# Kernel optimization log

Measured on AMD Instinct MI355X. Metric: run time of the kernel, lower is better.

## Reference

```python
import jax, jax.numpy as jnp
import numpy as np

N_HEADS = 16
DIM = 1024
HW = 32
B = 8


def _conv3x3(x, W, b):
    # x: [B, C, H, W], W: [O, I, 3, 3] (OIHW), padding 1 == SAME for stride 1
    y = jax.lax.conv_general_dilated(
        x, W, window_strides=(1, 1), padding='SAME',
        dimension_numbers=('NCHW', 'OIHW', 'NCHW'))
    return y + b[None, :, None, None]


def setup_inputs() -> dict:
    key = jax.random.key(0)
    ks = jax.random.split(key, 8)
    f32 = jnp.float32
    q = jax.random.normal(ks[0], (B, DIM, HW, HW), f32)
    k = jax.random.normal(ks[1], (B, DIM, HW, HW), f32)
    v = jax.random.normal(ks[2], (B, DIM, HW, HW), f32)
    Wq = jax.random.normal(ks[3], (DIM, DIM, 3, 3), f32) * 0.02
    Wk = jax.random.normal(ks[4], (DIM, DIM, 3, 3), f32) * 0.02
    Wv = jax.random.normal(ks[5], (DIM, DIM, 3, 3), f32) * 0.02
    Wo = jax.random.normal(ks[6], (DIM, DIM), f32) * 0.02
    bq = jnp.zeros((DIM,), f32); bk = jnp.zeros((DIM,), f32)
    bv = jnp.zeros((DIM,), f32); bo = jnp.zeros((DIM,), f32)
    mask = jax.random.randint(ks[7], (B, DIM, DIM), 0, 2, jnp.int32)
    return {'q': q, 'k': k, 'v': v, 'Wq': Wq, 'bq': bq, 'Wk': Wk, 'bk': bk,
            'Wv': Wv, 'bv': bv, 'Wo': Wo, 'bo': bo, 'mask': mask}


def reference(q, k, v, Wq, bq, Wk, bk, Wv, bv, Wo, bo, mask):
    Bq, C, H, W = q.shape  # C == dim, tokens = channels
    h = N_HEADS
    d = (H * W) // h  # head dim

    def split_heads(x):
        # [B, C, H, W] -> [B, h, C, d]
        return x.reshape(Bq, C, h, d).transpose(0, 2, 1, 3)

    qh = split_heads(_conv3x3(q, Wq, bq))
    kh = split_heads(_conv3x3(k, Wk, bk))
    vh = split_heads(_conv3x3(v, Wv, bv))

    scale = 1.0 / np.sqrt(d).astype(np.float32)
    attn = jnp.einsum('bhtd,bhsd->bhts', qh, kh) * scale  # [B, h, C, C]
    attn = jnp.where(mask[:, None, :, :] == 0, jnp.float32(-1e9), attn)
    w = jax.nn.softmax(attn, axis=-1)  # attn_dropout rate = 0 -> identity
    out = jnp.einsum('bhts,bhsd->bhtd', w, vh)  # [B, h, C, d]
    out = out.transpose(0, 2, 1, 3).reshape(Bq, C, h * d)  # [B, C, H*W]
    out = out @ Wo.T + bo  # Linear(dim, dim); H*W == dim
    return out
```

## Files before the change

kernel.cpp:

```cpp
#include <hip/hip_runtime.h>

typedef __attribute__((ext_vector_type(8))) short bh8;
typedef __attribute__((ext_vector_type(4))) short bh4;
typedef __attribute__((ext_vector_type(4))) float f32x4;

__device__ __forceinline__ short f2bf(float f) {
  union { float f; unsigned u; } a; a.f = f;
  unsigned r = a.u + 0x7FFFu + ((a.u >> 16) & 1u);
  return (short)(r >> 16);
}

__device__ __forceinline__ void g2l16(const short* g, short* l) {
  __builtin_amdgcn_global_load_lds(
      (const __attribute__((address_space(1))) void*)g,
      (__attribute__((address_space(3))) void*)l, 16, 0, 0);
}

__global__ __launch_bounds__(256) void zero_halo(short* __restrict__ xP) {
  int z = blockIdx.y;
  short* base = xP + (size_t)z * 1183744;
  int ri = blockIdx.x * 2 + (threadIdx.x >> 7);
  int row;
  if (ri < 34) row = ri;
  else if (ri < 68) row = 1122 + (ri - 34);
  else { int j = ri - 68; int y = (j >> 1) + 1; int x = (j & 1) ? 33 : 0; row = y * 34 + x; }
  int col = (threadIdx.x & 127) * 8;
  bh8 zv = {0, 0, 0, 0, 0, 0, 0, 0};
  *(bh8*)(base + (size_t)row * 1024 + col) = zv;
}

__global__ __launch_bounds__(256) void transpose3(
    const float* __restrict__ q, const float* __restrict__ k, const float* __restrict__ v,
    short* __restrict__ qP, short* __restrict__ kP, short* __restrict__ vP) {
  int z = blockIdx.z; int tensor = z >> 3, b = z & 7;
  const float* src = tensor == 0 ? q : (tensor == 1 ? k : v);
  short* dst = tensor == 0 ? qP : (tensor == 1 ? kP : vP);
  src += (size_t)b * 1048576; dst += (size_t)b * 1183744;
  int row0 = blockIdx.y * 64;
  int col0 = blockIdx.x * 64;
  __shared__ short t[64][72];
  int tid = threadIdx.x;
#pragma unroll
  for (int i = 0; i < 2; ++i) {
    int cid = tid + i * 256;
    int r = cid >> 3, co = (cid & 7) * 8;
    const float* p = src + (size_t)(row0 + r) * 1024 + col0 + co;
    float4 f0 = *(const float4*)(p);
    float4 f1 = *(const float4*)(p + 4);
    t[co + 0][r] = f2bf(f0.x); t[co + 1][r] = f2bf(f0.y);
    t[co + 2][r] = f2bf(f0.z); t[co + 3][r] = f2bf(f0.w);
    t[co + 4][r] = f2bf(f1.x); t[co + 5][r] = f2bf(f1.y);
    t[co + 6][r] = f2bf(f1.z); t[co + 7][r] = f2bf(f1.w);
  }
  __syncthreads();
#pragma unroll
  for (int i = 0; i < 2; ++i) {
    int cid = tid + i * 256;
    int sr = cid >> 3, cc = (cid & 7) * 8;
    bh8 val = *(const bh8*)&t[sr][cc];
    int tok = col0 + sr;
    int pr = ((tok >> 5) + 1) * 34 + (tok & 31) + 1;
    *(bh8*)(dst + (size_t)pr * 1024 + row0 + cc) = val;
  }
}

__global__ __launch_bounds__(256) void wperm3(
    const float* __restrict__ Wq, const float* __restrict__ Wk, const float* __restrict__ Wv,
    short* __restrict__ WpQ, short* __restrict__ WpK, short* __restrict__ WpV) {
  int z = blockIdx.y;
  const float* W = z == 0 ? Wq : (z == 1 ? Wk : Wv);
  short* Wp = z == 0 ? WpQ : (z == 1 ? WpK : WpV);
  int idx = blockIdx.x * 256 + threadIdx.x;
  const float* wsrc = W + (size_t)idx * 9;
#pragma unroll
  for (int t = 0; t < 9; ++t) Wp[(size_t)t * 1048576 + idx] = f2bf(wsrc[t]);
}

__global__ __launch_bounds__(256) void cvt_bf(const float* __restrict__ src,
                                              short* __restrict__ dst) {
  int idx = (blockIdx.x * 256 + threadIdx.x) * 4;
  float4 f = *(const float4*)(src + idx);
  bh4 o; o[0] = f2bf(f.x); o[1] = f2bf(f.y); o[2] = f2bf(f.z); o[3] = f2bf(f.w);
  *(bh4*)(dst + idx) = o;
}

__global__ __launch_bounds__(256) void mask_pack(const int* __restrict__ m,
                                                 unsigned* __restrict__ mp) {
  int idx = blockIdx.x * 256 + threadIdx.x;
  const int* src = m + (size_t)idx * 32;
  unsigned wv = 0;
#pragma unroll
  for (int j = 0; j < 32; j += 4) {
    int4 a = *(const int4*)(src + j);
    wv |= ((unsigned)(a.x & 1) << j) | ((unsigned)(a.y & 1) << (j + 1)) |
          ((unsigned)(a.z & 1) << (j + 2)) | ((unsigned)(a.w & 1) << (j + 3));
  }
  mp[idx] = wv;
}

__global__ __launch_bounds__(256) void conv_gemm_all(
    const short* __restrict__ WpQ, const short* __restrict__ WpK, const short* __restrict__ WpV,
    const short* __restrict__ xPq, const short* __restrict__ xPk, const short* __restrict__ xPv,
    short* __restrict__ cQ, short* __restrict__ cK, short* __restrict__ cVT,
    const float* __restrict__ bq, const float* __restrict__ bk, const float* __restrict__ bv,
    int convSel) {
  __shared__ short sA[4096];
  __shared__ short sB[4096];
  int tid = threadIdx.x, lane = tid & 63, w = tid >> 6;
  int z = blockIdx.z;
  int conv = convSel >= 0 ? convSel : (z >> 3);
  int b = convSel >= 0 ? z : (z & 7);
  const short* Wp = conv == 0 ? WpQ : (conv == 1 ? WpK : WpV);
  const short* xP = conv == 0 ? xPq : (conv == 1 ? xPk : xPv);
  short* out = conv == 0 ? cQ : (conv == 1 ? cK : cVT);
  const float* bias = conv == 0 ? bq : (conv == 1 ? bk : bv);
  int XisA = (conv == 2);
  int mbase = blockIdx.x * 128, nbase = blockIdx.y * 128;
  const short* xb = xP + (size_t)b * 1183744;
  int wbase = XisA ? nbase : mbase;
  int sbase = XisA ? mbase : nbase;
  short* sW = XisA ? sB : sA;
  short* sX = XisA ? sA : sB;

  int colsh = (lane & 3) * 8;
  int ldsoff[2]; const short* wp0[2]; const short* xp0[2];
#pragma unroll
  for (int i = 0; i < 2; ++i) {
    int row = 32 * w + 16 * i + (lane >> 2);
    ldsoff[i] = (2 * w + i) * 512 + lane * 8;
    wp0[i] = Wp + (size_t)(wbase + row) * 1024 + colsh;
    int tok = sbase + row;
    int pr0 = ((tok >> 5) + 1) * 34 + (tok & 31) + 1;
    xp0[i] = xb + (size_t)pr0 * 1024 + colsh;
  }
  f32x4 acc[4][4] = {};
  int wm = (w >> 1) * 64, wn = (w & 1) * 64;
  for (int tap = 0; tap < 9; ++tap) {
    int dOff = (tap / 3 - 1) * 34 + (tap % 3 - 1);
    size_t wtap = (size_t)tap * 1048576;
    for (int kt = 0; kt < 1024; kt += 32) {
#pragma unroll
      for (int i = 0; i < 2; ++i) {
        g2l16(wp0[i] + wtap + kt, sW + ldsoff[i]);
        g2l16(xp0[i] + (ptrdiff_t)dOff * 1024 + kt, sX + ldsoff[i]);
      }
      __syncthreads();
      bh8 af[4], bfr[4];
#pragma unroll
      for (int mt = 0; mt < 4; ++mt)
        af[mt] = *(const bh8*)&sA[(wm + mt * 16 + (lane & 15)) * 32 + (lane >> 4) * 8];
#pragma unroll
      for (int nt = 0; nt < 4; ++nt)
        bfr[nt] = *(const bh8*)&sB[(wn + nt * 16 + (lane & 15)) * 32 + (lane >> 4) * 8];
#pragma unroll
      for (int mt = 0; mt < 4; ++mt)
#pragma unroll
        for (int nt = 0; nt < 4; ++nt)
          acc[mt][nt] = __builtin_amdgcn_mfma_f32_16x16x32_bf16(af[mt], bfr[nt], acc[mt][nt], 0, 0, 0);
      __syncthreads();
    }
  }
  size_t ob = (size_t)b * 1048576;
#pragma unroll
  for (int mt = 0; mt < 4; ++mt) {
#pragma unroll
    for (int nt = 0; nt < 4; ++nt) {
      int m0 = mbase + wm + mt * 16 + ((lane >> 4) << 2);
      int n = nbase + wn + nt * 16 + (lane & 15);
#pragma unroll
      for (int r = 0; r < 4; ++r) {
        float bv = bias[XisA ? n : (m0 + r)];
        out[ob + (size_t)(m0 + r) * 1024 + n] = f2bf(acc[mt][nt][r] + bv);
      }
    }
  }
}

__global__ __launch_bounds__(256) void attn(
    const short* __restrict__ Qc, const short* __restrict__ Kc,
    const short* __restrict__ VT, const unsigned* __restrict__ Mp,
    short* __restrict__ AO) {
  __shared__ short sQ[64][72];
  __shared__ short sK[128][72];
  __shared__ short sV[64][136];
  __shared__ short sP[64][136];
  int tid = threadIdx.x, lane = tid & 63, w = tid >> 6;
  int qbase = blockIdx.x * 64, h = blockIdx.y, b = blockIdx.z;
  int j0 = h * 64;
  const short* Qb = Qc + (size_t)b * 1048576;
  const short* Kb = Kc + (size_t)b * 1048576;
  const short* Vb = VT + (size_t)b * 1048576;
  const unsigned* Mpb = Mp + (size_t)b * 32768;
  const float scale = 0.125f;

#pragma unroll
  for (int i = 0; i < 2; ++i) {
    int cid = tid + i * 256;
    int row = cid >> 3, co = (cid & 7) * 8;
    *(bh8*)&sQ[row][co] = *(const bh8*)(Qb + (size_t)(qbase + row) * 1024 + j0 + co);
  }
  __syncthreads();

  int tg = qbase + w * 16 + (lane & 15);
  int rsel = ((lane >> 4) << 2);
  float mrow = -3.0e38f, lrow = 0.0f;
  f32x4 oacc[4] = {};

  for (int st = 0; st < 8; ++st) {
#pragma unroll
    for (int i = 0; i < 4; ++i) {
      int cid = tid + i * 256;
      int row = cid >> 3, co = (cid & 7) * 8;
      *(bh8*)&sK[row][co] = *(const bh8*)(Kb + (size_t)(st * 128 + row) * 1024 + j0 + co);
      int vrow = cid >> 4, vco = (cid & 15) * 8;
      *(bh8*)&sV[vrow][vco] = *(const bh8*)(Vb + (size_t)(j0 + vrow) * 1024 + st * 128 + vco);
    }
    __syncthreads();

    f32x4 sacc[8];
#pragma unroll
    for (int mt = 0; mt < 8; ++mt) {
      f32x4 a = {0.f, 0.f, 0.f, 0.f};
      bh8 kf = *(const bh8*)&sK[mt * 16 + (lane & 15)][(lane >> 4) * 8];
      bh8 qf = *(const bh8*)&sQ[w * 16 + (lane & 15)][(lane >> 4) * 8];
      a = __builtin_amdgcn_mfma_f32_16x16x32_bf16(kf, qf, a, 0, 0, 0);
      kf = *(const bh8*)&sK[mt * 16 + (lane & 15)][32 + (lane >> 4) * 8];
      qf = *(const bh8*)&sQ[w * 16 + (lane & 15)][32 + (lane >> 4) * 8];
      a = __builtin_amdgcn_mfma_f32_16x16x32_bf16(kf, qf, a, 0, 0, 0);
      sacc[mt] = a;
    }

    uint4 Mw = *(const uint4*)(Mpb + (size_t)tg * 32 + st * 4);
    float tmax = -3.0e38f;
#pragma unroll
    for (int mt = 0; mt < 8; ++mt) {
      unsigned mwv = ((const unsigned*)&Mw)[mt >> 1] >> ((mt & 1) * 16 + rsel);
      f32x4 vv;
      vv[0] = (mwv & 1u) ? sacc[mt][0] * scale : -1e9f;
      vv[1] = (mwv & 2u) ? sacc[mt][1] * scale : -1e9f;
      vv[2] = (mwv & 4u) ? sacc[mt][2] * scale : -1e9f;
      vv[3] = (mwv & 8u) ? sacc[mt][3] * scale : -1e9f;
      sacc[mt] = vv;
      tmax = fmaxf(tmax, fmaxf(fmaxf(vv[0], vv[1]), fmaxf(vv[2], vv[3])));
    }
    tmax = fmaxf(tmax, __shfl_xor(tmax, 16, 64));
    tmax = fmaxf(tmax, __shfl_xor(tmax, 32, 64));
    float mnew = fmaxf(mrow, tmax);
    float alpha = __expf(fminf(mrow - mnew, 0.f));

    float sum = 0.f;
    uint4 Mw2 = Mw;
#pragma unroll
    for (int mt = 0; mt < 8; ++mt) {
      unsigned mwv = ((const unsigned*)&Mw2)[mt >> 1] >> ((mt & 1) * 16 + rsel);
      float p0 = (mwv & 1u) ? __expf(fminf(sacc[mt][0] - mnew, 0.f)) : 0.f;
      float p1 = (mwv & 2u) ? __expf(fminf(sacc[mt][1] - mnew, 0.f)) : 0.f;
      float p2 = (mwv & 4u) ? __expf(fminf(sacc[mt][2] - mnew, 0.f)) : 0.f;
      float p3 = (mwv & 8u) ? __expf(fminf(sacc[mt][3] - mnew, 0.f)) : 0.f;
      sum += (p0 + p1) + (p2 + p3);
      bh4 p; p[0] = f2bf(p0); p[1] = f2bf(p1); p[2] = f2bf(p2); p[3] = f2bf(p3);
      *(bh4*)&sP[w * 16 + (lane & 15)][mt * 16 + rsel] = p;
    }
    sum += __shfl_xor(sum, 16, 64);
    sum += __shfl_xor(sum, 32, 64);
    lrow = lrow * alpha + sum;
    mrow = mnew;

    float al[4];
#pragma unroll
    for (int r = 0; r < 4; ++r) al[r] = __shfl(alpha, rsel + r, 64);
#pragma unroll
    for (int nt = 0; nt < 4; ++nt)
#pragma unroll
      for (int r = 0; r < 4; ++r) oacc[nt][r] *= al[r];
    __syncthreads();

#pragma unroll
    for (int k0 = 0; k0 < 4; ++k0) {
      bh8 pf = *(const bh8*)&sP[w * 16 + (lane & 15)][k0 * 32 + (lane >> 4) * 8];
#pragma unroll
      for (int nt = 0; nt < 4; ++nt) {
        bh8 vf = *(const bh8*)&sV[nt * 16 + (lane & 15)][k0 * 32 + (lane >> 4) * 8];
        oacc[nt] = __builtin_amdgcn_mfma_f32_16x16x32_bf16(pf, vf, oacc[nt], 0, 0, 0);
      }
    }
    __syncthreads();
  }

  float rl[4];
#pragma unroll
  for (int r = 0; r < 4; ++r) rl[r] = 1.0f / __shfl(lrow, rsel + r, 64);
  size_t ob = (size_t)b * 1048576;
#pragma unroll
  for (int nt = 0; nt < 4; ++nt) {
    int j = nt * 16 + (lane & 15);
    int t0 = qbase + w * 16 + rsel;
#pragma unroll
    for (int r = 0; r < 4; ++r)
      AO[ob + (size_t)(t0 + r) * 1024 + j0 + j] = f2bf(oacc[nt][r] * rl[r]);
  }
}

__global__ __launch_bounds__(256) void gemm_bt(
    const short* __restrict__ A, const short* __restrict__ Bm,
    float* __restrict__ out, const float* __restrict__ bias) {
  __shared__ short sA[4096];
  __shared__ short sB[4096];
  int tid = threadIdx.x, lane = tid & 63, w = tid >> 6;
  int mbase = blockIdx.x * 128, nbase = blockIdx.y * 128;
  int colsh = (lane & 3) * 8;
  int ldsoff[2]; const short* ap[2]; const short* bp[2];
#pragma unroll
  for (int i = 0; i < 2; ++i) {
    int row = 32 * w + 16 * i + (lane >> 2);
    ldsoff[i] = (2 * w + i) * 512 + lane * 8;
    ap[i] = A + (size_t)(mbase + row) * 1024 + colsh;
    bp[i] = Bm + (size_t)(nbase + row) * 1024 + colsh;
  }
  f32x4 acc[4][4] = {};
  int wm = (w >> 1) * 64, wn = (w & 1) * 64;
  for (int kt = 0; kt < 1024; kt += 32) {
#pragma unroll
    for (int i = 0; i < 2; ++i) {
      g2l16(ap[i] + kt, sA + ldsoff[i]);
      g2l16(bp[i] + kt, sB + ldsoff[i]);
    }
    __syncthreads();
    bh8 af[4], bfr[4];
#pragma unroll
    for (int mt = 0; mt < 4; ++mt)
      af[mt] = *(const bh8*)&sA[(wm + mt * 16 + (lane & 15)) * 32 + (lane >> 4) * 8];
#pragma unroll
    for (int nt = 0; nt < 4; ++nt)
      bfr[nt] = *(const bh8*)&sB[(wn + nt * 16 + (lane & 15)) * 32 + (lane >> 4) * 8];
#pragma unroll
    for (int mt = 0; mt < 4; ++mt)
#pragma unroll
      for (int nt = 0; nt < 4; ++nt)
        acc[mt][nt] = __builtin_amdgcn_mfma_f32_16x16x32_bf16(af[mt], bfr[nt], acc[mt][nt], 0, 0, 0);
    __syncthreads();
  }
#pragma unroll
  for (int mt = 0; mt < 4; ++mt) {
#pragma unroll
    for (int nt = 0; nt < 4; ++nt) {
      int m0 = mbase + wm + mt * 16 + ((lane >> 4) << 2);
      int n = nbase + wn + nt * 16 + (lane & 15);
      float bv = bias[n];
#pragma unroll
      for (int r = 0; r < 4; ++r)
        out[(size_t)(m0 + r) * 1024 + n] = acc[mt][nt][r] + bv;
    }
  }
}

extern "C" void kernel_launch(void* const* d_in, const int* in_sizes, int n_in,
                              void* d_out, int out_size, void* d_ws, size_t ws_size,
                              hipStream_t stream) {
  (void)in_sizes; (void)n_in; (void)out_size;
  const float* q    = (const float*)d_in[0];
  const float* k    = (const float*)d_in[1];
  const float* v    = (const float*)d_in[2];
  const float* Wq   = (const float*)d_in[3];
  const float* bq   = (const float*)d_in[4];
  const float* Wk   = (const float*)d_in[5];
  const float* bk   = (const float*)d_in[6];
  const float* Wv   = (const float*)d_in[7];
  const float* bv   = (const float*)d_in[8];
  const float* Wo   = (const float*)d_in[9];
  const float* bo   = (const float*)d_in[10];
  const int*   mask = (const int*)d_in[11];
  float* out = (float*)d_out;
  char* ws = (char*)d_ws;

  const size_t XPE = 1156ull * 1024 * 8;
  const size_t XPB = XPE * 2;
  const size_t WPE = 9ull * 1048576;
  short* xPq = (short*)ws;
  short* xPk = xPq + XPE;
  short* xPv = xPk + XPE;
  short* WpQ = (short*)(ws + 3 * XPB);
  short* WpK = WpQ + WPE;
  short* WpV = WpK + WPE;
  char* p2 = ws + 3 * XPB + 3 * WPE * 2;

  bool fused = ws_size >= 167000000ull;
  short *cQ, *cK, *cVT, *WoB, *AO; unsigned* Mpk;
  if (fused) {
    cQ  = (short*)(p2);
    cK  = (short*)(p2 + 16777216);
    cVT = (short*)(p2 + 33554432);
    WoB = (short*)(p2 + 50331648);
    Mpk = (unsigned*)(p2 + 52428800);
    AO  = xPq;
  } else {
    cQ  = (short*)(p2);
    WoB = (short*)(p2 + 16777216);
    Mpk = (unsigned*)(p2 + 18874368);
    cK  = xPq;
    cVT = xPk;
    AO  = xPv;
  }

  zero_halo<<<dim3(66, 24), dim3(256), 0, stream>>>(xPq);
  transpose3<<<dim3(16, 16, 24), dim3(256), 0, stream>>>(q, k, v, xPq, xPk, xPv);
  wperm3<<<dim3(4096, 3), dim3(256), 0, stream>>>(Wq, Wk, Wv, WpQ, WpK, WpV);
  cvt_bf<<<dim3(1024), dim3(256), 0, stream>>>(Wo, WoB);
  mask_pack<<<dim3(1024), dim3(256), 0, stream>>>(mask, Mpk);
  if (fused) {
    conv_gemm_all<<<dim3(8, 8, 24), dim3(256), 0, stream>>>(
        WpQ, WpK, WpV, xPq, xPk, xPv, cQ, cK, cVT, bq, bk, bv, -1);
  } else {
    conv_gemm_all<<<dim3(8, 8, 8), dim3(256), 0, stream>>>(
        WpQ, WpK, WpV, xPq, xPk, xPv, cQ, cK, cVT, bq, bk, bv, 0);
    conv_gemm_all<<<dim3(8, 8, 8), dim3(256), 0, stream>>>(
        WpQ, WpK, WpV, xPq, xPk, xPv, cQ, cK, cVT, bq, bk, bv, 1);
    conv_gemm_all<<<dim3(8, 8, 8), dim3(256), 0, stream>>>(
        WpQ, WpK, WpV, xPq, xPk, xPv, cQ, cK, cVT, bq, bk, bv, 2);
  }
  attn<<<dim3(16, 16, 8), dim3(256), 0, stream>>>(cQ, cK, cVT, Mpk, AO);
  gemm_bt<<<dim3(64, 8), dim3(256), 0, stream>>>(AO, WoB, out, bo);
}
```

Before: 913.8 us.

## Rewrite conv GEMM as 256x256 tile, 4-stage LDS pipeline with swizzle

Replaces the 128x128 single-buffered conv implicit-GEMM with a 512-thread kernel that computes 256x256 tiles. It uses a 4-deep LDS ring of global_load_lds stages with explicit vmcnt waits, raw barriers, and setprio around MFMA bursts. The LDS column layout is XOR-swizzled to avoid bank conflicts, and workgroup IDs are remapped so neighbouring blocks share operands in cache. This aims to hide global load latency and raise arithmetic intensity, which matters because the conv GEMMs dominate runtime. In exchange it uses 128 KB of LDS and many accumulator registers per wave, with a correctness risk from the manual waitcnt accounting.

```diff
diff --git a/kernel.cpp b/kernel.cpp
--- a/kernel.cpp
+++ b/kernel.cpp
@@ -14,6 +14,12 @@
   __builtin_amdgcn_global_load_lds(
       (const __attribute__((address_space(1))) void*)g,
       (__attribute__((address_space(3))) void*)l, 16, 0, 0);
+}
+
+__device__ __forceinline__ void barrier_raw() {
+  asm volatile("" ::: "memory");
+  __builtin_amdgcn_s_barrier();
+  asm volatile("" ::: "memory");
 }
 
 __global__ __launch_bounds__(256) void zero_halo(short* __restrict__ xP) {
@@ -98,16 +104,21 @@
   mp[idx] = wv;
 }
 
-__global__ __launch_bounds__(256) void conv_gemm_all(
+__global__ __launch_bounds__(512, 2) void conv_gemm256(
     const short* __restrict__ WpQ, const short* __restrict__ WpK, const short* __restrict__ WpV,
     const short* __restrict__ xPq, const short* __restrict__ xPk, const short* __restrict__ xPv,
     short* __restrict__ cQ, short* __restrict__ cK, short* __restrict__ cVT,
     const float* __restrict__ bq, const float* __restrict__ bk, const float* __restrict__ bv,
     int convSel) {
-  __shared__ short sA[4096];
-  __shared__ short sB[4096];
-  int tid = threadIdx.x, lane = tid & 63, w = tid >> 6;
-  int z = blockIdx.z;
+  __shared__ short lds[65536];
+  int tid = threadIdx.x, lane = tid & 63, wid = tid >> 6;
+
+  int fid = blockIdx.x + (blockIdx.y << 2) + (blockIdx.z << 4);
+  int nwg = (int)(gridDim.z) << 4;
+  int cpx = nwg >> 3;
+  int swz = (fid & 7) * cpx + (fid >> 3);
+  int mtile = swz & 3, ntile = (swz >> 2) & 3, z = swz >> 4;
+
   int conv = convSel >= 0 ? convSel : (z >> 3);
   int b = convSel >= 0 ? z : (z & 7);
   const short* Wp = conv == 0 ? WpQ : (conv == 1 ? WpK : WpV);
@@ -115,62 +126,119 @@
   short* out = conv == 0 ? cQ : (conv == 1 ? cK : cVT);
   const float* bias = conv == 0 ? bq : (conv == 1 ? bk : bv);
   int XisA = (conv == 2);
-  int mbase = blockIdx.x * 128, nbase = blockIdx.y * 128;
+  int mbase = mtile * 256, nbase = ntile * 256;
   const short* xb = xP + (size_t)b * 1183744;
   int wbase = XisA ? nbase : mbase;
   int sbase = XisA ? mbase : nbase;
-  short* sW = XisA ? sB : sA;
-  short* sX = XisA ? sA : sB;
-
-  int colsh = (lane & 3) * 8;
-  int ldsoff[2]; const short* wp0[2]; const short* xp0[2];
-#pragma unroll
-  for (int i = 0; i < 2; ++i) {
-    int row = 32 * w + 16 * i + (lane >> 2);
-    ldsoff[i] = (2 * w + i) * 512 + lane * 8;
-    wp0[i] = Wp + (size_t)(wbase + row) * 1024 + colsh;
-    int tok = sbase + row;
-    int pr0 = ((tok >> 5) + 1) * 34 + (tok & 31) + 1;
-    xp0[i] = xb + (size_t)pr0 * 1024 + colsh;
-  }
-  f32x4 acc[4][4] = {};
-  int wm = (w >> 1) * 64, wn = (w & 1) * 64;
-  for (int tap = 0; tap < 9; ++tap) {
-    int dOff = (tap / 3 - 1) * 34 + (tap % 3 - 1);
-    size_t wtap = (size_t)tap * 1048576;
-    for (int kt = 0; kt < 1024; kt += 32) {
-#pragma unroll
-      for (int i = 0; i < 2; ++i) {
-        g2l16(wp0[i] + wtap + kt, sW + ldsoff[i]);
-        g2l16(xp0[i] + (ptrdiff_t)dOff * 1024 + kt, sX + ldsoff[i]);
-      }
-      __syncthreads();
-      bh8 af[4], bfr[4];
-#pragma unroll
-      for (int mt = 0; mt < 4; ++mt)
-        af[mt] = *(const bh8*)&sA[(wm + mt * 16 + (lane & 15)) * 32 + (lane >> 4) * 8];
-#pragma unroll
-      for (int nt = 0; nt < 4; ++nt)
-        bfr[nt] = *(const bh8*)&sB[(wn + nt * 16 + (lane & 15)) * 32 + (lane >> 4) * 8];
-#pragma unroll
-      for (int mt = 0; mt < 4; ++mt)
-#pragma unroll
-        for (int nt = 0; nt < 4; ++nt)
-          acc[mt][nt] = __builtin_amdgcn_mfma_f32_16x16x32_bf16(af[mt], bfr[nt], acc[mt][nt], 0, 0, 0);
-      __syncthreads();
-    }
-  }
+
+  int srow = wid * 16 + (lane >> 2);
+  int lsl = (lane & 3) ^ ((lane >> 2) & 3);
+  int gcol = lsl * 8;
+  const short* pW[2]; const short* pX[2];
+#pragma unroll
+  for (int h = 0; h < 2; ++h) {
+    pW[h] = Wp + (size_t)(wbase + h * 128 + srow) * 1024 + gcol;
+    int tok = sbase + h * 128 + srow;
+    int pr = ((tok >> 5) + 1) * 34 + (tok & 31) + 1;
+    pX[h] = xb + (size_t)pr * 1024 + gcol;
+  }
+  const short* pA0 = XisA ? pX[0] : pW[0];
+  const short* pA1 = XisA ? pX[1] : pW[1];
+  const short* pB0 = XisA ? pW[0] : pX[0];
+  const short* pB1 = XisA ? pW[1] : pX[1];
+  int sdst = wid * 512 + lane * 8;
+
+  int pslot = (((lane >> 4) ^ (lane & 3)) << 3);
+  int rdA = ((wid >> 2) * 128 + (lane & 15)) * 32 + pslot;
+  int rdB = 8192 + ((wid & 3) * 64 + (lane & 15)) * 32 + pslot;
+
+  f32x4 acc[8][4] = {};
+  short* stBd = nullptr; const short* stBs0 = nullptr; const short* stBs1 = nullptr;
+
+#pragma unroll
+  for (int u = 0; u < 3; ++u) {
+    ptrdiff_t dW = (ptrdiff_t)(u << 5);
+    ptrdiff_t dX = (ptrdiff_t)(-35) * 1024 + (u << 5);
+    ptrdiff_t dA = XisA ? dX : dW, dB = XisA ? dW : dX;
+    short* du = &lds[u * 16384 + sdst];
+    g2l16(pA0 + dA, du);
+    g2l16(pA1 + dA, du + 4096);
+    g2l16(pB0 + dB, du + 8192);
+    g2l16(pB1 + dB, du + 12288);
+  }
+  asm volatile("s_waitcnt vmcnt(8)" ::: "memory");
+  barrier_raw();
+
+#define CT_MFMA16(ACCROW) \
+    _Pragma("unroll") for (int mm = 0; mm < 4; ++mm) { \
+      _Pragma("unroll") for (int nn = 0; nn < 4; ++nn) \
+        acc[(ACCROW) + mm][nn] = __builtin_amdgcn_mfma_f32_16x16x32_bf16( \
+            afr[mm], bfr[nn], acc[(ACCROW) + mm][nn], 0, 0, 0); \
+    }
+
+#define TILEBODY(REGS, T, DOSTAGE, WSTR) do { \
+    const short* Lp = &lds[(REGS)]; \
+    bh8 afr[4], bfr[4]; \
+    _Pragma("unroll") for (int mm = 0; mm < 4; ++mm) \
+      afr[mm] = *(const bh8*)(Lp + rdA + mm * 512); \
+    _Pragma("unroll") for (int nn = 0; nn < 4; ++nn) \
+      bfr[nn] = *(const bh8*)(Lp + rdB + nn * 512); \
+    if (DOSTAGE) { \
+      int u_ = (T) + 3; \
+      int tap_ = u_ >> 5, kk_ = (u_ & 31) << 5; \
+      int tapr_ = (tap_ * 11) >> 5; \
+      ptrdiff_t dW_ = (ptrdiff_t)tap_ * 1048576 + kk_; \
+      ptrdiff_t dX_ = (ptrdiff_t)(tapr_ * 34 + (tap_ - tapr_ * 3) - 35) * 1024 + kk_; \
+      ptrdiff_t dA_ = XisA ? dX_ : dW_, dB_ = XisA ? dW_ : dX_; \
+      short* du_ = &lds[(u_ & 3) * 16384 + sdst]; \
+      g2l16(pA0 + dA_, du_); \
+      g2l16(pA1 + dA_, du_ + 4096); \
+      stBd = du_ + 8192; stBs0 = pB0 + dB_; stBs1 = pB1 + dB_; \
+    } \
+    barrier_raw(); \
+    __builtin_amdgcn_s_setprio(1); \
+    CT_MFMA16(0) \
+    __builtin_amdgcn_s_setprio(0); \
+    barrier_raw(); \
+    _Pragma("unroll") for (int mm = 0; mm < 4; ++mm) \
+      afr[mm] = *(const bh8*)(Lp + rdA + 2048 + mm * 512); \
+    if (DOSTAGE) { g2l16(stBs0, stBd); g2l16(stBs1, stBd + 4096); } \
+    barrier_raw(); \
+    __builtin_amdgcn_s_setprio(1); \
+    CT_MFMA16(4) \
+    __builtin_amdgcn_s_setprio(0); \
+    asm volatile(WSTR ::: "memory"); \
+    barrier_raw(); \
+  } while (0)
+
+#pragma unroll 1
+  for (int it = 0; it < 71; ++it) {
+    int t0 = it * 4;
+#pragma unroll
+    for (int j = 0; j < 4; ++j) {
+      TILEBODY(j * 16384, t0 + j, true, "s_waitcnt vmcnt(8)");
+    }
+  }
+  TILEBODY(0,     284, true,  "s_waitcnt vmcnt(8)");
+  TILEBODY(16384, 285, false, "s_waitcnt vmcnt(4)");
+  TILEBODY(32768, 286, false, "s_waitcnt vmcnt(0)");
+  TILEBODY(49152, 287, false, "");
+
+#undef TILEBODY
+#undef CT_MFMA16
+
   size_t ob = (size_t)b * 1048576;
-#pragma unroll
-  for (int mt = 0; mt < 4; ++mt) {
-#pragma unroll
-    for (int nt = 0; nt < 4; ++nt) {
-      int m0 = mbase + wm + mt * 16 + ((lane >> 4) << 2);
-      int n = nbase + wn + nt * 16 + (lane & 15);
+  int wr = wid >> 2, wc = wid & 3;
+#pragma unroll
+  for (int m = 0; m < 8; ++m) {
+#pragma unroll
+    for (int n = 0; n < 4; ++n) {
+      int m0 = mbase + wr * 128 + m * 16 + ((lane >> 4) << 2);
+      int nn = nbase + wc * 64 + n * 16 + (lane & 15);
 #pragma unroll
       for (int r = 0; r < 4; ++r) {
-        float bv = bias[XisA ? n : (m0 + r)];
-        out[ob + (size_t)(m0 + r) * 1024 + n] = f2bf(acc[mt][nt][r] + bv);
+        float bvv = bias[XisA ? nn : (m0 + r)];
+        out[ob + (size_t)(m0 + r) * 1024 + nn] = f2bf(acc[m][n][r] + bvv);
       }
     }
   }
@@ -408,14 +476,14 @@
   cvt_bf<<<dim3(1024), dim3(256), 0, stream>>>(Wo, WoB);
   mask_pack<<<dim3(1024), dim3(256), 0, stream>>>(mask, Mpk);
   if (fused) {
-    conv_gemm_all<<<dim3(8, 8, 24), dim3(256), 0, stream>>>(
+    conv_gemm256<<<dim3(4, 4, 24), dim3(512), 0, stream>>>(
         WpQ, WpK, WpV, xPq, xPk, xPv, cQ, cK, cVT, bq, bk, bv, -1);
   } else {
-    conv_gemm_all<<<dim3(8, 8, 8), dim3(256), 0, stream>>>(
+    conv_gemm256<<<dim3(4, 4, 8), dim3(512), 0, stream>>>(
         WpQ, WpK, WpV, xPq, xPk, xPv, cQ, cK, cVT, bq, bk, bv, 0);
-    conv_gemm_all<<<dim3(8, 8, 8), dim3(256), 0, stream>>>(
+    conv_gemm256<<<dim3(4, 4, 8), dim3(512), 0, stream>>>(
         WpQ, WpK, WpV, xPq, xPk, xPv, cQ, cK, cVT, bq, bk, bv, 1);
-    conv_gemm_all<<<dim3(8, 8, 8), dim3(256), 0, stream>>>(
+    conv_gemm256<<<dim3(4, 4, 8), dim3(512), 0, stream>>>(
         WpQ, WpK, WpV, xPq, xPk, xPv, cQ, cK, cVT, bq, bk, bv, 2);
   }
   attn<<<dim3(16, 16, 8), dim3(256), 0, stream>>>(cQ, cK, cVT, Mpk, AO);
```

Result: faster. 891.9 us (-2.4%).

## Rewrite conv GEMM with triple-buffered LDS pipeline, larger tiles and swizzle

Applied to the files above, without the earlier changes.

Replaces the conv implicit-GEMM kernel with a 512-thread, 256x128-tile version. It prefetches two k-steps ahead into three rotating LDS buffers, waits with vmcnt and uses one raw barrier per step. It also XOR-swizzles LDS slots to cut bank conflicts, raises wave priority during MFMAs, and remaps block ids so neighbouring tiles share a chiplet. The aim is to hide global-load latency and cut barrier stalls, at the cost of more LDS per block and lower occupancy.

```diff
diff --git a/kernel.cpp b/kernel.cpp
--- a/kernel.cpp
+++ b/kernel.cpp
@@ -14,6 +14,12 @@
   __builtin_amdgcn_global_load_lds(
       (const __attribute__((address_space(1))) void*)g,
       (__attribute__((address_space(3))) void*)l, 16, 0, 0);
+}
+
+__device__ __forceinline__ void barrier_raw() {
+  asm volatile("" ::: "memory");
+  __builtin_amdgcn_s_barrier();
+  asm volatile("" ::: "memory");
 }
 
 __global__ __launch_bounds__(256) void zero_halo(short* __restrict__ xP) {
@@ -98,16 +104,21 @@
   mp[idx] = wv;
 }
 
-__global__ __launch_bounds__(256) void conv_gemm_all(
+__global__ __launch_bounds__(512, 4) void conv_gemm_td(
     const short* __restrict__ WpQ, const short* __restrict__ WpK, const short* __restrict__ WpV,
     const short* __restrict__ xPq, const short* __restrict__ xPk, const short* __restrict__ xPv,
     short* __restrict__ cQ, short* __restrict__ cK, short* __restrict__ cVT,
     const float* __restrict__ bq, const float* __restrict__ bk, const float* __restrict__ bv,
     int convSel) {
-  __shared__ short sA[4096];
-  __shared__ short sB[4096];
-  int tid = threadIdx.x, lane = tid & 63, w = tid >> 6;
-  int z = blockIdx.z;
+  __shared__ short lds[36864];
+  int tid = threadIdx.x, lane = tid & 63, wid = tid >> 6;
+
+  int fid = blockIdx.x + (blockIdx.y << 2) + ((int)blockIdx.z << 5);
+  int nwg = (int)gridDim.z << 5;
+  int cpx = nwg >> 3;
+  int swz = (fid & 7) * cpx + (fid >> 3);
+  int mtile = swz & 3, ntile = (swz >> 2) & 7, z = swz >> 5;
+
   int conv = convSel >= 0 ? convSel : (z >> 3);
   int b = convSel >= 0 ? z : (z & 7);
   const short* Wp = conv == 0 ? WpQ : (conv == 1 ? WpK : WpV);
@@ -115,62 +126,95 @@
   short* out = conv == 0 ? cQ : (conv == 1 ? cK : cVT);
   const float* bias = conv == 0 ? bq : (conv == 1 ? bk : bv);
   int XisA = (conv == 2);
-  int mbase = blockIdx.x * 128, nbase = blockIdx.y * 128;
+  int mbase = mtile * 256, nbase = ntile * 128;
   const short* xb = xP + (size_t)b * 1183744;
-  int wbase = XisA ? nbase : mbase;
-  int sbase = XisA ? mbase : nbase;
-  short* sW = XisA ? sB : sA;
-  short* sX = XisA ? sA : sB;
-
-  int colsh = (lane & 3) * 8;
-  int ldsoff[2]; const short* wp0[2]; const short* xp0[2];
-#pragma unroll
-  for (int i = 0; i < 2; ++i) {
-    int row = 32 * w + 16 * i + (lane >> 2);
-    ldsoff[i] = (2 * w + i) * 512 + lane * 8;
-    wp0[i] = Wp + (size_t)(wbase + row) * 1024 + colsh;
-    int tok = sbase + row;
-    int pr0 = ((tok >> 5) + 1) * 34 + (tok & 31) + 1;
-    xp0[i] = xb + (size_t)pr0 * 1024 + colsh;
-  }
+
+  int srow = tid >> 2;
+  int lsl = (tid & 3) ^ ((tid >> 3) & 3);
+  int gcol = lsl * 8;
+  const short* pA0; const short* pA1; const short* pB0;
+  if (!XisA) {
+    pA0 = Wp + (size_t)(mbase + srow) * 1024 + gcol;
+    pA1 = Wp + (size_t)(mbase + 128 + srow) * 1024 + gcol;
+    int tok = nbase + srow;
+    pB0 = xb + (size_t)(((tok >> 5) + 1) * 34 + (tok & 31) + 1) * 1024 + gcol;
+  } else {
+    int ta = mbase + srow, tb = mbase + 128 + srow;
+    pA0 = xb + (size_t)(((ta >> 5) + 1) * 34 + (ta & 31) + 1) * 1024 + gcol;
+    pA1 = xb + (size_t)(((tb >> 5) + 1) * 34 + (tb & 31) + 1) * 1024 + gcol;
+    pB0 = Wp + (size_t)(nbase + srow) * 1024 + gcol;
+  }
+  int sdst = tid * 8;
+
+  int pslot = (((lane >> 4) ^ ((lane >> 1) & 3)) << 3);
+  int wr = wid >> 1, wc = wid & 1;
+  int rdA = (wr * 64 + (lane & 15)) * 32 + pslot;
+  int rdB = 8192 + (wc * 64 + (lane & 15)) * 32 + pslot;
+
   f32x4 acc[4][4] = {};
-  int wm = (w >> 1) * 64, wn = (w & 1) * 64;
-  for (int tap = 0; tap < 9; ++tap) {
-    int dOff = (tap / 3 - 1) * 34 + (tap % 3 - 1);
-    size_t wtap = (size_t)tap * 1048576;
-    for (int kt = 0; kt < 1024; kt += 32) {
-#pragma unroll
-      for (int i = 0; i < 2; ++i) {
-        g2l16(wp0[i] + wtap + kt, sW + ldsoff[i]);
-        g2l16(xp0[i] + (ptrdiff_t)dOff * 1024 + kt, sX + ldsoff[i]);
-      }
-      __syncthreads();
-      bh8 af[4], bfr[4];
-#pragma unroll
-      for (int mt = 0; mt < 4; ++mt)
-        af[mt] = *(const bh8*)&sA[(wm + mt * 16 + (lane & 15)) * 32 + (lane >> 4) * 8];
-#pragma unroll
-      for (int nt = 0; nt < 4; ++nt)
-        bfr[nt] = *(const bh8*)&sB[(wn + nt * 16 + (lane & 15)) * 32 + (lane >> 4) * 8];
-#pragma unroll
-      for (int mt = 0; mt < 4; ++mt)
-#pragma unroll
-        for (int nt = 0; nt < 4; ++nt)
-          acc[mt][nt] = __builtin_amdgcn_mfma_f32_16x16x32_bf16(af[mt], bfr[nt], acc[mt][nt], 0, 0, 0);
-      __syncthreads();
-    }
-  }
+
+#define STAGE(U, SRB) do { \
+    int u_ = (U); \
+    int tap_ = u_ >> 5, kk_ = (u_ & 31) << 5; \
+    int ty_ = (tap_ * 11) >> 5; \
+    ptrdiff_t dW_ = (ptrdiff_t)tap_ * 1048576 + kk_; \
+    ptrdiff_t dX_ = (ptrdiff_t)(ty_ * 34 + (tap_ - ty_ * 3) - 35) * 1024 + kk_; \
+    ptrdiff_t dA_ = XisA ? dX_ : dW_, dB_ = XisA ? dW_ : dX_; \
+    short* du_ = &lds[(SRB) + sdst]; \
+    g2l16(pA0 + dA_, du_); \
+    g2l16(pA1 + dA_, du_ + 4096); \
+    g2l16(pB0 + dB_, du_ + 8192); \
+  } while (0)
+
+  STAGE(0, 0);
+  STAGE(1, 12288);
+  asm volatile("s_waitcnt vmcnt(3)" ::: "memory");
+  barrier_raw();
+
+#define TILEBODY(RB, T, DOSTAGE, SRB, WSTR) do { \
+    const short* Lp = &lds[(RB)]; \
+    bh8 afr[4], bfr[4]; \
+    _Pragma("unroll") for (int mt = 0; mt < 4; ++mt) \
+      afr[mt] = *(const bh8*)(Lp + rdA + mt * 512); \
+    _Pragma("unroll") for (int nt = 0; nt < 4; ++nt) \
+      bfr[nt] = *(const bh8*)(Lp + rdB + nt * 512); \
+    if (DOSTAGE) STAGE((T) + 2, SRB); \
+    __builtin_amdgcn_s_setprio(1); \
+    _Pragma("unroll") for (int mt = 0; mt < 4; ++mt) { \
+      _Pragma("unroll") for (int nt = 0; nt < 4; ++nt) \
+        acc[mt][nt] = __builtin_amdgcn_mfma_f32_16x16x32_bf16( \
+            afr[mt], bfr[nt], acc[mt][nt], 0, 0, 0); \
+    } \
+    __builtin_amdgcn_s_setprio(0); \
+    asm volatile(WSTR ::: "memory"); \
+    barrier_raw(); \
+  } while (0)
+
+#pragma unroll 1
+  for (int it = 0; it < 95; ++it) {
+    int t0 = it * 3;
+    TILEBODY(0,     t0 + 0, true, 24576, "s_waitcnt vmcnt(3)");
+    TILEBODY(12288, t0 + 1, true, 0,     "s_waitcnt vmcnt(3)");
+    TILEBODY(24576, t0 + 2, true, 12288, "s_waitcnt vmcnt(3)");
+  }
+  TILEBODY(0,     285, true,  24576, "s_waitcnt vmcnt(3)");
+  TILEBODY(12288, 286, false, 0,     "s_waitcnt vmcnt(0)");
+  TILEBODY(24576, 287, false, 0,     "");
+
+#undef TILEBODY
+#undef STAGE
+
   size_t ob = (size_t)b * 1048576;
 #pragma unroll
   for (int mt = 0; mt < 4; ++mt) {
 #pragma unroll
     for (int nt = 0; nt < 4; ++nt) {
-      int m0 = mbase + wm + mt * 16 + ((lane >> 4) << 2);
-      int n = nbase + wn + nt * 16 + (lane & 15);
+      int m0 = mbase + wr * 64 + mt * 16 + ((lane >> 4) << 2);
+      int nn = nbase + wc * 64 + nt * 16 + (lane & 15);
 #pragma unroll
       for (int r = 0; r < 4; ++r) {
-        float bv = bias[XisA ? n : (m0 + r)];
-        out[ob + (size_t)(m0 + r) * 1024 + n] = f2bf(acc[mt][nt][r] + bv);
+        float bvv = bias[XisA ? nn : (m0 + r)];
+        out[ob + (size_t)(m0 + r) * 1024 + nn] = f2bf(acc[mt][nt][r] + bvv);
       }
     }
   }
@@ -408,14 +452,14 @@
   cvt_bf<<<dim3(1024), dim3(256), 0, stream>>>(Wo, WoB);
   mask_pack<<<dim3(1024), dim3(256), 0, stream>>>(mask, Mpk);
   if (fused) {
-    conv_gemm_all<<<dim3(8, 8, 24), dim3(256), 0, stream>>>(
+    conv_gemm_td<<<dim3(4, 8, 24), dim3(512), 0, stream>>>(
         WpQ, WpK, WpV, xPq, xPk, xPv, cQ, cK, cVT, bq, bk, bv, -1);
   } else {
-    conv_gemm_all<<<dim3(8, 8, 8), dim3(256), 0, stream>>>(
+    conv_gemm_td<<<dim3(4, 8, 8), dim3(512), 0, stream>>>(
         WpQ, WpK, WpV, xPq, xPk, xPv, cQ, cK, cVT, bq, bk, bv, 0);
-    conv_gemm_all<<<dim3(8, 8, 8), dim3(256), 0, stream>>>(
+    conv_gemm_td<<<dim3(4, 8, 8), dim3(512), 0, stream>>>(
         WpQ, WpK, WpV, xPq, xPk, xPv, cQ, cK, cVT, bq, bk, bv, 1);
-    conv_gemm_all<<<dim3(8, 8, 8), dim3(256), 0, stream>>>(
+    conv_gemm_td<<<dim3(4, 8, 8), dim3(512), 0, stream>>>(
         WpQ, WpK, WpV, xPq, xPk, xPv, cQ, cK, cVT, bq, bk, bv, 2);
   }
   attn<<<dim3(16, 16, 8), dim3(256), 0, stream>>>(cQ, cK, cVT, Mpk, AO);
```

After: 805.7 us. -11.8%, faster.
